# Optimization experiments

Measured on AMD Instinct MI355X. Metric: run time of the kernel, lower is better.

The kernel has to match this reference:

```python
import jax, jax.numpy as jnp
import numpy as np

NUM_HEADS = 16
ROTARY_BASE = 10000.0


def _rope_cos_sin(seqlen, rotary_dim, dtype):
    # inv_freq: (rotary_dim/2,), cos/sin: (seqlen, rotary_dim/2)
    inv_freq = 1.0 / (ROTARY_BASE ** (jnp.arange(0, rotary_dim, 2, dtype=jnp.float32) / rotary_dim))
    t = jnp.arange(seqlen, dtype=jnp.float32)
    freqs = jnp.outer(t, inv_freq)
    return jnp.cos(freqs).astype(dtype), jnp.sin(freqs).astype(dtype)


def _apply_rotary(x, cos, sin):
    # x: (b, s, h, d); cos/sin: (s, d/2). Non-interleaved (GPT-NeoX) halves.
    d2 = cos.shape[-1]
    x1, x2 = x[..., :d2], x[..., d2:2 * d2]
    c = cos[None, :, None, :]
    s = sin[None, :, None, :]
    r1 = x1 * c - x2 * s
    r2 = x1 * s + x2 * c
    return jnp.concatenate([r1, r2], axis=-1)


def setup_inputs() -> dict:
    key = jax.random.key(0)
    ks = jax.random.split(key, 5)
    B, S, E = 2, 2048, 2048
    x = jax.random.normal(ks[0], (B, S, E), dtype=jnp.float32)
    wqkv_w = jax.random.normal(ks[1], (3 * E, E), dtype=jnp.float32) * 0.02
    wqkv_b = jax.random.normal(ks[2], (3 * E,), dtype=jnp.float32) * 0.02
    out_w = jax.random.normal(ks[3], (E, E), dtype=jnp.float32) * 0.02
    out_b = jax.random.normal(ks[4], (E,), dtype=jnp.float32) * 0.02
    return {"x": x, "wqkv_w": wqkv_w, "wqkv_b": wqkv_b, "out_w": out_w, "out_b": out_b}


def reference(x, wqkv_w, wqkv_b, out_w, out_b):
    B, S, E = x.shape
    H = NUM_HEADS
    D = E // H
    # fused QKV projection: (b, s, 3, h, d)
    qkv = (jnp.einsum('bse,fe->bsf', x, wqkv_w) + wqkv_b).reshape(B, S, 3, H, D)
    q, k, v = qkv[:, :, 0], qkv[:, :, 1], qkv[:, :, 2]
    # rotary embedding on full head_dim of q and k
    cos, sin = _rope_cos_sin(S, D, x.dtype)
    q = _apply_rotary(q, cos, sin)
    k = _apply_rotary(k, cos, sin)
    # causal self-attention, softmax_scale = 1/sqrt(head_dim)
    scale = 1.0 / jnp.sqrt(jnp.asarray(D, dtype=x.dtype))
    scores = jnp.einsum('bshd,bthd->bhst', q, k) * scale
    causal_mask = jnp.tril(jnp.ones((S, S), dtype=bool))
    scores = jnp.where(causal_mask[None, None], scores, jnp.asarray(-1e30, dtype=scores.dtype))
    attn = jax.nn.softmax(scores, axis=-1)
    ctx = jnp.einsum('bhst,bthd->bshd', attn, v).reshape(B, S, E)
    return jnp.einsum('bse,fe->bsf', ctx, out_w) + out_b
```

## Files before the change

### kernel.cpp

```cpp
#include <hip/hip_runtime.h>

typedef unsigned short u16;
typedef unsigned int u32;
typedef __bf16 bf16x8 __attribute__((ext_vector_type(8)));
typedef float fx4 __attribute__((ext_vector_type(4)));

__device__ __forceinline__ float bf2f(u16 u) {
    return __uint_as_float(((u32)u) << 16);
}
__device__ __forceinline__ u16 f2bf(float f) {
    u32 x = __float_as_uint(f);
    u32 r = (x + 0x7fffu + ((x >> 16) & 1u)) >> 16;
    return (u16)r;
}

__device__ __forceinline__ void gld16(const u16* g, u16* l) {
    __builtin_amdgcn_global_load_lds(
        (const __attribute__((address_space(1))) void*)g,
        (__attribute__((address_space(3))) void*)l, 16, 0, 0);
}

#define MFMA16(a, b, c) __builtin_amdgcn_mfma_f32_16x16x32_bf16((a), (b), (c), 0, 0, 0)

__global__ __launch_bounds__(256) void cvt_kernel(const float* __restrict__ x,
                                                  const float* __restrict__ w1,
                                                  const float* __restrict__ w2,
                                                  u16* __restrict__ xb,
                                                  u16* __restrict__ w1b,
                                                  u16* __restrict__ w2b) {
    size_t g = ((size_t)blockIdx.x * 256 + threadIdx.x) * 8;
    const float* src;
    u16* dst;
    if (g < 8388608) {
        src = x;
        dst = xb;
    } else if (g < 20971520) {
        src = w1 - 8388608;
        dst = w1b - 8388608;
    } else {
        src = w2 - 20971520;
        dst = w2b - 20971520;
    }
    float4 a = *(const float4*)&src[g];
    float4 b = *(const float4*)&src[g + 4];
    u16 v[8];
    v[0] = f2bf(a.x);
    v[1] = f2bf(a.y);
    v[2] = f2bf(a.z);
    v[3] = f2bf(a.w);
    v[4] = f2bf(b.x);
    v[5] = f2bf(b.y);
    v[6] = f2bf(b.z);
    v[7] = f2bf(b.w);
    *(uint4*)&dst[g] = *(const uint4*)v;
}

template <int MODE>
__global__ __launch_bounds__(256, 2) void gemm_bt(const u16* __restrict__ A,
                                                  const u16* __restrict__ B,
                                                  const float* __restrict__ bias,
                                                  float* __restrict__ Cf,
                                                  u16* __restrict__ qb,
                                                  u16* __restrict__ kb,
                                                  u16* __restrict__ vb,
                                                  int N, int K) {
    __shared__ __align__(16) u16 As[128 * 32];
    __shared__ __align__(16) u16 Bs[128 * 32];

    const int tid = threadIdx.x;
    const int lane = tid & 63;
    const int wave = tid >> 6;
    const int quad = lane >> 4;
    const int m16 = lane & 15;
    const int wm = wave >> 1, wn = wave & 1;
    const int bm = blockIdx.y * 128, bn = blockIdx.x * 128;

    const int r0 = tid >> 2;
    const int u0 = (tid & 3) ^ ((r0 >> 1) & 3);
    const int r1 = (tid + 256) >> 2;
    const int u1 = ((tid + 256) & 3) ^ ((r1 >> 1) & 3);
    const u16* a0 = &A[(size_t)(bm + r0) * K + u0 * 8];
    const u16* a1 = &A[(size_t)(bm + r1) * K + u1 * 8];
    const u16* b0 = &B[(size_t)(bn + r0) * K + u0 * 8];
    const u16* b1 = &B[(size_t)(bn + r1) * K + u1 * 8];
    u16* la0 = &As[tid * 8];
    u16* la1 = &As[(tid + 256) * 8];
    u16* lb0 = &Bs[tid * 8];
    u16* lb1 = &Bs[(tid + 256) * 8];

    const int su = (quad ^ ((m16 >> 1) & 3)) * 8;

    const fx4 zero4 = {0.f, 0.f, 0.f, 0.f};
    fx4 acc[4][4];
#pragma unroll
    for (int i = 0; i < 4; ++i)
#pragma unroll
        for (int j = 0; j < 4; ++j) acc[i][j] = zero4;

    const int nk = K >> 5;
    for (int kt = 0; kt < nk; ++kt) {
        const int k0 = kt << 5;
        gld16(a0 + k0, la0);
        gld16(a1 + k0, la1);
        gld16(b0 + k0, lb0);
        gld16(b1 + k0, lb1);
        __syncthreads();
        bf16x8 af[4], bfr[4];
#pragma unroll
        for (int t = 0; t < 4; ++t) {
            af[t] = *(const bf16x8*)&As[(wm * 64 + t * 16 + m16) * 32 + su];
            bfr[t] = *(const bf16x8*)&Bs[(wn * 64 + t * 16 + m16) * 32 + su];
        }
#pragma unroll
        for (int mt = 0; mt < 4; ++mt)
#pragma unroll
            for (int nt = 0; nt < 4; ++nt)
                acc[mt][nt] = MFMA16(af[mt], bfr[nt], acc[mt][nt]);
        __syncthreads();
    }

#pragma unroll
    for (int mt = 0; mt < 4; ++mt) {
#pragma unroll
        for (int r = 0; r < 4; ++r) {
            int row = bm + wm * 64 + mt * 16 + quad * 4 + r;
#pragma unroll
            for (int nt = 0; nt < 4; ++nt) {
                int col = bn + wn * 64 + nt * 16 + m16;
                float v = acc[mt][nt][r] + bias[col];
                if (MODE == 0) {
                    Cf[(size_t)row * N + col] = v;
                } else {
                    int which = col >> 11;
                    int h = (col >> 7) & 15;
                    int d = col & 127;
                    int b = row >> 11;
                    int s = row & 2047;
                    u16* dst = (which == 0) ? qb : ((which == 1) ? kb : vb);
                    dst[(size_t)((b * 16 + h) * 2048 + s) * 128 + d] = f2bf(v);
                }
            }
        }
    }
}

__global__ __launch_bounds__(256) void rope_kernel(u16* __restrict__ q,
                                                   u16* __restrict__ k) {
    int t = blockIdx.x * 256 + threadIdx.x;
    int i = t & 63;
    int s = (t >> 6) & 2047;
    int bh = t >> 17;
    float inv = exp2f(-(float)i * 0.2076205059304595f);
    float ang = (float)s * inv;
    float sn, cs;
    sincosf(ang, &sn, &cs);
    size_t base = ((size_t)bh * 2048 + s) * 128 + i;
    {
        float x1 = bf2f(q[base]), x2 = bf2f(q[base + 64]);
        q[base] = f2bf(x1 * cs - x2 * sn);
        q[base + 64] = f2bf(x1 * sn + x2 * cs);
    }
    {
        float x1 = bf2f(k[base]), x2 = bf2f(k[base + 64]);
        k[base] = f2bf(x1 * cs - x2 * sn);
        k[base + 64] = f2bf(x1 * sn + x2 * cs);
    }
}

__global__ __launch_bounds__(256) void vtrans_kernel(const u16* __restrict__ v,
                                                     u16* __restrict__ vt) {
    __shared__ __align__(16) u16 L[128 * 66];
    const int tid = threadIdx.x;
    const int kb = blockIdx.x * 64;
    const int bh = blockIdx.y;
    const u16* vp = v + (size_t)bh * 2048 * 128;
    u16* op = vt + (size_t)bh * 128 * 2048;
#pragma unroll
    for (int i = 0; i < 4; ++i) {
        int c = i * 256 + tid;
        int t = c >> 4, d8 = (c & 15) << 3;
        uint4 x = *(const uint4*)&vp[(kb + t) * 128 + d8];
        const u16* xs = (const u16*)&x;
#pragma unroll
        for (int j = 0; j < 8; ++j) L[(d8 + j) * 66 + t] = xs[j];
    }
    __syncthreads();
#pragma unroll
    for (int i = 0; i < 4; ++i) {
        int c = i * 256 + tid;
        int d = c >> 3, t8 = (c & 7) << 3;
        uint4 x;
        u16* xs = (u16*)&x;
#pragma unroll
        for (int j = 0; j < 8; ++j) xs[j] = L[d * 66 + t8 + j];
        *(uint4*)&op[(size_t)d * 2048 + kb + t8] = x;
    }
}

__global__ __launch_bounds__(256, 2) void attn_kernel(const u16* __restrict__ q,
                                                      const u16* __restrict__ k,
                                                      const u16* __restrict__ vt,
                                                      u16* __restrict__ ctx) {
    __shared__ __align__(16) u16 Ks[2][64 * 128];
    __shared__ __align__(16) u16 Vs[2][128 * 64];
    __shared__ __align__(16) u16 Ps[4][16 * 64];

    const int tid = threadIdx.x;
    const int lane = tid & 63;
    const int wave = tid >> 6;
    const int quad = lane >> 4;
    const int m16 = lane & 15;

    const int l = blockIdx.x;
    const int half0 = l & 1;
    const int qt0 = (l >> 1) & 7;
    const int bh = l >> 4;
    const int b = bh >> 4, h = bh & 15;
    const u16* qp = q + (size_t)bh * 2048 * 128;
    const u16* kp = k + (size_t)bh * 2048 * 128;
    const u16* vp = vt + (size_t)bh * 128 * 2048;
    const float scale = 0.08838834764831845f;
    const fx4 zero4 = {0.f, 0.f, 0.f, 0.f};

    int ksrc[4], vsrc[4];
#pragma unroll
    for (int i = 0; i < 4; ++i) {
        int s = tid + i * 256;
        int r = s >> 4, p = s & 15;
        ksrc[i] = r * 128 + (p ^ (r & 7)) * 8;
        int d = s >> 3, pv = s & 7;
        vsrc[i] = d * 2048 + (pv ^ (d & 7)) * 8;
    }

#define GLD_TILE(kb_, buf_)                                                   \
    {                                                                         \
        _Pragma("unroll") for (int ii = 0; ii < 4; ++ii) {                    \
            gld16(kp + (size_t)(kb_)*128 + ksrc[ii],                          \
                  &Ks[buf_][tid * 8 + ii * 2048]);                            \
            gld16(vp + (kb_) + vsrc[ii], &Vs[buf_][tid * 8 + ii * 2048]);     \
        }                                                                     \
    }

#pragma unroll 1
    for (int pass = 0; pass < 2; ++pass) {
        const int qt = pass ? (15 - qt0) : qt0;
        const int hf = pass ? (1 - half0) : half0;
        const int qrow0 = qt * 128 + hf * 64 + wave * 16;
        const int nkt = 2 * qt + 1 + hf;

        bf16x8 qf[4];
#pragma unroll
        for (int c = 0; c < 4; ++c)
            qf[c] = *(const bf16x8*)&qp[(size_t)(qrow0 + m16) * 128 + c * 32 +
                                        quad * 8];

        fx4 o[8];
#pragma unroll
        for (int dn = 0; dn < 8; ++dn) o[dn] = zero4;
        float mi[4], li[4];
#pragma unroll
        for (int r = 0; r < 4; ++r) {
            mi[r] = -1e30f;
            li[r] = 0.f;
        }

        GLD_TILE(0, 0);
        __syncthreads();
        int cur = 0;
        for (int kt = 0; kt < nkt; ++kt) {
            const int kb = kt * 64;
            if (kt + 1 < nkt) GLD_TILE(kb + 64, cur ^ 1);

            fx4 sc[4];
#pragma unroll
            for (int nt = 0; nt < 4; ++nt) sc[nt] = zero4;
            __builtin_amdgcn_s_setprio(1);
#pragma unroll
            for (int c = 0; c < 4; ++c)
#pragma unroll
                for (int nt = 0; nt < 4; ++nt) {
                    int e = (nt * 16 + m16) * 128 + c * 32 + quad * 8;
                    bf16x8 kf =
                        *(const bf16x8*)&Ks[cur][e ^ ((m16 & 7) << 3)];
                    sc[nt] = MFMA16(qf[c], kf, sc[nt]);
                }
            __builtin_amdgcn_s_setprio(0);

#pragma unroll
            for (int r = 0; r < 4; ++r) {
                int rg = qrow0 + quad * 4 + r;
                float mx = mi[r];
#pragma unroll
                for (int nt = 0; nt < 4; ++nt) {
                    int cg = kb + nt * 16 + m16;
                    float s = sc[nt][r] * scale;
                    s = (cg <= rg) ? s : -1e30f;
                    sc[nt][r] = s;
                    mx = fmaxf(mx, s);
                }
                mx = fmaxf(mx, __shfl_xor(mx, 1));
                mx = fmaxf(mx, __shfl_xor(mx, 2));
                mx = fmaxf(mx, __shfl_xor(mx, 4));
                mx = fmaxf(mx, __shfl_xor(mx, 8));
                float alpha = __expf(mi[r] - mx);
                mi[r] = mx;
                float rsum = 0.f;
                int row = quad * 4 + r;
#pragma unroll
                for (int nt = 0; nt < 4; ++nt) {
                    float p = __expf(sc[nt][r] - mx);
                    Ps[wave][(row * 64 + nt * 16 + m16) ^ ((row & 7) << 3)] =
                        f2bf(p);
                    rsum += p;
                }
                rsum += __shfl_xor(rsum, 1);
                rsum += __shfl_xor(rsum, 2);
                rsum += __shfl_xor(rsum, 4);
                rsum += __shfl_xor(rsum, 8);
                li[r] = li[r] * alpha + rsum;
#pragma unroll
                for (int dn = 0; dn < 8; ++dn) o[dn][r] *= alpha;
            }

            __builtin_amdgcn_s_setprio(1);
#pragma unroll
            for (int c2 = 0; c2 < 2; ++c2) {
                bf16x8 pf = *(const bf16x8*)&Ps[wave][(m16 * 64 + c2 * 32 +
                                                       quad * 8) ^
                                                      ((m16 & 7) << 3)];
#pragma unroll
                for (int dn = 0; dn < 8; ++dn) {
                    int e = (dn * 16 + m16) * 64 + c2 * 32 + quad * 8;
                    bf16x8 vf =
                        *(const bf16x8*)&Vs[cur][e ^ ((m16 & 7) << 3)];
                    o[dn] = MFMA16(pf, vf, o[dn]);
                }
            }
            __builtin_amdgcn_s_setprio(0);

            __syncthreads();
            cur ^= 1;
        }

#pragma unroll
        for (int r = 0; r < 4; ++r) {
            int row = qrow0 + quad * 4 + r;
            float inv = 1.0f / li[r];
#pragma unroll
            for (int dn = 0; dn < 8; ++dn) {
                int d = dn * 16 + m16;
                ctx[((size_t)(b * 2048 + row)) * 2048 + h * 128 + d] =
                    f2bf(o[dn][r] * inv);
            }
        }
    }
}

extern "C" void kernel_launch(void* const* d_in, const int* in_sizes, int n_in,
                              void* d_out, int out_size, void* d_ws,
                              size_t ws_size, hipStream_t stream) {
    const float* x = (const float*)d_in[0];
    const float* wqkv_w = (const float*)d_in[1];
    const float* wqkv_b = (const float*)d_in[2];
    const float* out_w = (const float*)d_in[3];
    const float* out_b = (const float*)d_in[4];
    u16* ws = (u16*)d_ws;

    u16* xb = ws;
    u16* wqkvb = ws + 8388608;
    u16* vb = ws + 20971520;
    u16* outwb = ws + 29360128;
    u16* vtb = xb;
    u16* ctx = vb;
    u16* qb = (u16*)d_out;
    u16* kb = qb + 8388608;

    cvt_kernel<<<12288, 256, 0, stream>>>(x, wqkv_w, out_w, xb, wqkvb, outwb);
    gemm_bt<1><<<dim3(48, 32), 256, 0, stream>>>(xb, wqkvb, wqkv_b, nullptr,
                                                 qb, kb, vb, 6144, 2048);
    rope_kernel<<<16384, 256, 0, stream>>>(qb, kb);
    vtrans_kernel<<<dim3(32, 32), 256, 0, stream>>>(vb, vtb);
    attn_kernel<<<512, 256, 0, stream>>>(qb, kb, vtb, ctx);
    gemm_bt<0><<<dim3(16, 32), 256, 0, stream>>>(ctx, outwb, out_b,
                                                 (float*)d_out, nullptr,
                                                 nullptr, nullptr, 2048, 2048);
}
```

Measured before the change: 424.1 us.

## Double-buffer LDS tiles in bf16 GEMM with async prefetch two steps ahead

The GEMM's LDS tiles are now double-buffered. Global-to-LDS loads for tile k+2 are issued after tile k has been consumed, with explicit vmcnt waits so one tile is always in flight while MFMAs run on the other. The MFMA block is also wrapped in s_setprio so the compute phase gets scheduling priority. This hides global load latency that the old load-sync-compute-sync loop exposed, at the cost of twice the LDS per block, which could lower occupancy, and hand-written waitcnt and barrier logic that must stay correct.

```diff
diff --git a/kernel.cpp b/kernel.cpp
--- a/kernel.cpp
+++ b/kernel.cpp
@@ -64,8 +64,8 @@
                                                   u16* __restrict__ kb,
                                                   u16* __restrict__ vb,
                                                   int N, int K) {
-    __shared__ __align__(16) u16 As[128 * 32];
-    __shared__ __align__(16) u16 Bs[128 * 32];
+    __shared__ __align__(16) u16 As[2][128 * 32];
+    __shared__ __align__(16) u16 Bs[2][128 * 32];
 
     const int tid = threadIdx.x;
     const int lane = tid & 63;
@@ -83,12 +83,17 @@
     const u16* a1 = &A[(size_t)(bm + r1) * K + u1 * 8];
     const u16* b0 = &B[(size_t)(bn + r0) * K + u0 * 8];
     const u16* b1 = &B[(size_t)(bn + r1) * K + u1 * 8];
-    u16* la0 = &As[tid * 8];
-    u16* la1 = &As[(tid + 256) * 8];
-    u16* lb0 = &Bs[tid * 8];
-    u16* lb1 = &Bs[(tid + 256) * 8];
 
     const int su = (quad ^ ((m16 >> 1) & 3)) * 8;
+
+#define GLDT(kt_, buf_)                                                       \
+    {                                                                         \
+        const int k0_ = (kt_) << 5;                                           \
+        gld16(a0 + k0_, &As[buf_][tid * 8]);                                  \
+        gld16(a1 + k0_, &As[buf_][(tid + 256) * 8]);                          \
+        gld16(b0 + k0_, &Bs[buf_][tid * 8]);                                  \
+        gld16(b1 + k0_, &Bs[buf_][(tid + 256) * 8]);                          \
+    }
 
     const fx4 zero4 = {0.f, 0.f, 0.f, 0.f};
     fx4 acc[4][4];
@@ -98,25 +103,42 @@
         for (int j = 0; j < 4; ++j) acc[i][j] = zero4;
 
     const int nk = K >> 5;
+    GLDT(0, 0);
+    if (nk > 1) {
+        GLDT(1, 1);
+        asm volatile("s_waitcnt vmcnt(4)" ::: "memory");
+    } else {
+        asm volatile("s_waitcnt vmcnt(0)" ::: "memory");
+    }
+    __builtin_amdgcn_s_barrier();
+
+    int cur = 0;
     for (int kt = 0; kt < nk; ++kt) {
-        const int k0 = kt << 5;
-        gld16(a0 + k0, la0);
-        gld16(a1 + k0, la1);
-        gld16(b0 + k0, lb0);
-        gld16(b1 + k0, lb1);
-        __syncthreads();
         bf16x8 af[4], bfr[4];
 #pragma unroll
         for (int t = 0; t < 4; ++t) {
-            af[t] = *(const bf16x8*)&As[(wm * 64 + t * 16 + m16) * 32 + su];
-            bfr[t] = *(const bf16x8*)&Bs[(wn * 64 + t * 16 + m16) * 32 + su];
-        }
+            af[t] = *(const bf16x8*)&As[cur][(wm * 64 + t * 16 + m16) * 32 + su];
+            bfr[t] = *(const bf16x8*)&Bs[cur][(wn * 64 + t * 16 + m16) * 32 + su];
+        }
+        __builtin_amdgcn_s_setprio(1);
 #pragma unroll
         for (int mt = 0; mt < 4; ++mt)
 #pragma unroll
             for (int nt = 0; nt < 4; ++nt)
                 acc[mt][nt] = MFMA16(af[mt], bfr[nt], acc[mt][nt]);
-        __syncthreads();
+        __builtin_amdgcn_s_setprio(0);
+        __builtin_amdgcn_sched_barrier(0);
+        asm volatile("s_waitcnt lgkmcnt(0)" ::: "memory");
+        __builtin_amdgcn_s_barrier();
+
+        if (kt + 2 < nk) {
+            GLDT(kt + 2, cur);
+            asm volatile("s_waitcnt vmcnt(4)" ::: "memory");
+        } else {
+            asm volatile("s_waitcnt vmcnt(0)" ::: "memory");
+        }
+        __builtin_amdgcn_s_barrier();
+        cur ^= 1;
     }
 
 #pragma unroll
```

Measured after the change: 415.0 us. 1.02x faster.
